# Kernel tuning notes

Hardware: AMD Instinct MI355X
Metric: run time of the kernel (lower is better)

Reference implementation:

```python
import jax, jax.numpy as jnp
import numpy as np

N = 100000   # nodes
E = 1600000  # edges per view
B = 256      # graphs in batch
D = 128      # feature dim
H, C = 4, 32 # heads, per-head channels (H*C = 128)


def _seg_softmax(logits, seg, num_seg):
    # numerically stable softmax over segments (per-destination / per-graph)
    m = jax.ops.segment_max(logits, seg, num_segments=num_seg)
    e = jnp.exp(logits - m[seg])
    s = jax.ops.segment_sum(e, seg, num_segments=num_seg)
    return e / s[seg]


def _gat_conv(x, edge_index, W, att_src, att_dst, bias):
    # PyG GATConv with add_self_loops=True, concat heads
    n = x.shape[0]
    loop = jnp.arange(n, dtype=edge_index.dtype)
    src = jnp.concatenate([edge_index[0], loop])
    dst = jnp.concatenate([edge_index[1], loop])
    xh = (x @ W).reshape(n, H, C)                      # [N,H,C]
    a_src = jnp.einsum('nhc,hc->nh', xh, att_src)      # [N,H]
    a_dst = jnp.einsum('nhc,hc->nh', xh, att_dst)
    alpha = jax.nn.leaky_relu(a_src[src] + a_dst[dst], 0.2)   # [E+N,H]
    alpha = _seg_softmax(alpha, dst, n)
    msg = xh[src] * alpha[..., None]                   # [E+N,H,C]
    out = jax.ops.segment_sum(msg, dst, num_segments=n)
    return out.reshape(n, H * C) + bias


def _global_attention(h, batch, gate_W, gate_b):
    gate = (h @ gate_W + gate_b)[:, 0]                 # [N]
    a = _seg_softmax(gate, batch, B)
    return jax.ops.segment_sum(a[:, None] * h, batch, num_segments=B)  # [B,128]


def setup_inputs() -> dict:
    key = jax.random.key(0)
    ks = jax.random.split(key, 32)
    p = lambda k, shp: (jax.random.normal(k, shp, dtype=jnp.float32) * 0.05)
    inp = {
        'x': jax.random.normal(ks[0], (N, D), dtype=jnp.float32),
        'edge_index_ast': jax.random.randint(ks[1], (2, E), 0, N, dtype=jnp.int32),
        'edge_index_cfg': jax.random.randint(ks[2], (2, E), 0, N, dtype=jnp.int32),
        'edge_index_pdg': jax.random.randint(ks[3], (2, E), 0, N, dtype=jnp.int32),
        'batch': jnp.sort(jax.random.randint(ks[4], (N,), 0, B, dtype=jnp.int32)),
        'ln_g': jnp.ones((D,), jnp.float32),
        'ln_b': jnp.zeros((D,), jnp.float32),
        'proj_W': p(ks[5], (D, D)), 'proj_b': p(ks[6], (D,)),
        'W_ast': p(ks[7], (D, H * C)), 'att_src_ast': p(ks[8], (H, C)), 'att_dst_ast': p(ks[9], (H, C)), 'bias_ast': p(ks[10], (H * C,)),
        'W_cfg': p(ks[11], (D, H * C)), 'att_src_cfg': p(ks[12], (H, C)), 'att_dst_cfg': p(ks[13], (H, C)), 'bias_cfg': p(ks[14], (H * C,)),
        'W_pdg': p(ks[15], (D, H * C)), 'att_src_pdg': p(ks[16], (H, C)), 'att_dst_pdg': p(ks[17], (H, C)), 'bias_pdg': p(ks[18], (H * C,)),
        'gate_W': p(ks[19], (H * C, 1)), 'gate_b': p(ks[20], (1,)),
        'clf_W1': p(ks[21], (3 * H * C, 128)), 'clf_b1': p(ks[22], (128,)),
        'clf_W2': p(ks[23], (128, 1)), 'clf_b2': p(ks[24], (1,)),
    }
    return inp


def reference(x, edge_index_ast, edge_index_cfg, edge_index_pdg, batch,
              ln_g, ln_b, proj_W, proj_b,
              W_ast, att_src_ast, att_dst_ast, bias_ast,
              W_cfg, att_src_cfg, att_dst_cfg, bias_cfg,
              W_pdg, att_src_pdg, att_dst_pdg, bias_pdg,
              gate_W, gate_b, clf_W1, clf_b1, clf_W2, clf_b2):
    # LayerNorm + proj + LeakyReLU (dropout = eval/no-op)
    mu = jnp.mean(x, axis=-1, keepdims=True)
    var = jnp.var(x, axis=-1, keepdims=True)
    xn = (x - mu) * jax.lax.rsqrt(var + 1e-5) * ln_g + ln_b
    h0 = jax.nn.leaky_relu(xn @ proj_W + proj_b, 0.01)

    h_ast = jax.nn.elu(_gat_conv(h0, edge_index_ast, W_ast, att_src_ast, att_dst_ast, bias_ast))
    g_ast = _global_attention(h_ast, batch, gate_W, gate_b)
    h_cfg = jax.nn.elu(_gat_conv(h0, edge_index_cfg, W_cfg, att_src_cfg, att_dst_cfg, bias_cfg))
    g_cfg = _global_attention(h_cfg, batch, gate_W, gate_b)
    h_pdg = jax.nn.elu(_gat_conv(h0, edge_index_pdg, W_pdg, att_src_pdg, att_dst_pdg, bias_pdg))
    g_pdg = _global_attention(h_pdg, batch, gate_W, gate_b)

    combined = jnp.concatenate([g_ast, g_cfg, g_pdg], axis=1)  # [B, 384]
    hid = jax.nn.leaky_relu(combined @ clf_W1 + clf_b1, 0.01)
    return (hid @ clf_W2 + clf_b2).reshape(-1)                 # [B]
```

## Files before the change

### kernel.cpp

```cpp
#include <hip/hip_runtime.h>
#include <hip/hip_bf16.h>
#include <hip/hip_fp16.h>
#include <math.h>

#define NN 100000
#define EE 1600000
#define BB 256
#define NBUCK 391
#define PBLK 384
#define CH 4167
#define TOTB (3 * PBLK)
#define ROWS_PAD 100096
#define EPV (EE + NN)
#define LOG2E 1.442695041f

typedef short bf16x8 __attribute__((ext_vector_type(8)));
typedef float f32x4 __attribute__((ext_vector_type(4)));

__device__ __forceinline__ unsigned short f2bf(float f) {
    __hip_bfloat16 h = __float2bfloat16(f);
    return *(unsigned short*)&h;
}
__device__ __forceinline__ unsigned short f2h(float f) {
    __half h = __float2half(f);
    return *(unsigned short*)&h;
}
__device__ __forceinline__ float h2f(unsigned short u) {
    __half h = *(__half*)&u;
    return __half2float(h);
}

__global__ __launch_bounds__(256) void pack_wt(const float* __restrict__ W0,
                                               const float* __restrict__ W1,
                                               const float* __restrict__ W2,
                                               const float* __restrict__ W3,
                                               const float* __restrict__ ln_g,
                                               unsigned short* __restrict__ WT) {
    int which = blockIdx.y;
    const float* W = which == 0 ? W0 : which == 1 ? W1 : which == 2 ? W2 : W3;
    int i = blockIdx.x * 256 + threadIdx.x;
    int n = i >> 7, k = i & 127;
    float v = W[k * 128 + n];
    if (which == 0) v *= ln_g[k];
    WT[which * 16384 + i] = f2bf(v);
}

__global__ __launch_bounds__(128) void ln_consts(const float* __restrict__ W,
                                                 const float* __restrict__ g,
                                                 const float* __restrict__ b,
                                                 float* __restrict__ c12) {
    int n = threadIdx.x;
    float c1 = 0.f, c2 = 0.f;
    for (int k = 0; k < 128; k++) {
        float w = W[k * 128 + n];
        c1 = fmaf(g[k], w, c1);
        c2 = fmaf(b[k], w, c2);
    }
    c12[n] = c1;
    c12[128 + n] = c2;
}


__device__ __forceinline__ void hist_body(int bid, int tid,
                                          const int* __restrict__ e0,
                                          const int* __restrict__ e1,
                                          const int* __restrict__ e2,
                                          int* __restrict__ blockHistT) {
    int v = bid / PBLK, p = bid % PBLK;
    const int* ei = v == 0 ? e0 : v == 1 ? e1 : e2;
    __shared__ int h[NBUCK];
    for (int i = tid; i < NBUCK; i += 256) h[i] = 0;
    __syncthreads();
    int ea = p * CH, ebnd = min(EE, ea + CH);
    int e = ea + tid;
    for (; e + 768 < ebnd; e += 1024) {
        int d0 = ei[EE + e], d1 = ei[EE + e + 256];
        int d2 = ei[EE + e + 512], d3 = ei[EE + e + 768];
        atomicAdd(&h[((unsigned)d0) >> 8], 1);
        atomicAdd(&h[((unsigned)d1) >> 8], 1);
        atomicAdd(&h[((unsigned)d2) >> 8], 1);
        atomicAdd(&h[((unsigned)d3) >> 8], 1);
    }
    for (; e < ebnd; e += 256) atomicAdd(&h[((unsigned)ei[EE + e]) >> 8], 1);
    __syncthreads();
    for (int i = tid; i < NBUCK; i += 256) blockHistT[i * TOTB + bid] = h[i];
}

__device__ __forceinline__ void proj_body(int nb, int tid,
                                          const float* __restrict__ X,
                                          const unsigned short* __restrict__ WT,
                                          const float* __restrict__ c12,
                                          const float* __restrict__ pb,
                                          unsigned short* __restrict__ Out) {
    int w = tid >> 6, lane = tid & 63;
    int ln = lane & 15, oct = lane >> 4;
    int row0 = nb * 128 + w * 32;

    f32x4 acc[2][8];
    #pragma unroll
    for (int i = 0; i < 2; i++)
        #pragma unroll
        for (int j = 0; j < 8; j++) acc[i][j] = (f32x4){0.f, 0.f, 0.f, 0.f};

    const float* X0 = X + (size_t)min(row0 + ln, NN - 1) * 128;
    const float* X1 = X + (size_t)min(row0 + 16 + ln, NN - 1) * 128;
    const bf16x8* Wr = (const bf16x8*)(WT + (size_t)ln * 128);

    float s0 = 0.f, q0 = 0.f, s1 = 0.f, q1 = 0.f;
    #pragma unroll
    for (int kq = 0; kq < 4; kq++) {
        int koff = kq * 4 + oct;
        float4 xa = *(const float4*)(X0 + koff * 8);
        float4 xb = *(const float4*)(X0 + koff * 8 + 4);
        float4 ya = *(const float4*)(X1 + koff * 8);
        float4 yb = *(const float4*)(X1 + koff * 8 + 4);
        s0 += (xa.x + xa.y) + (xa.z + xa.w) + (xb.x + xb.y) + (xb.z + xb.w);
        q0 += xa.x * xa.x + xa.y * xa.y + xa.z * xa.z + xa.w * xa.w
            + xb.x * xb.x + xb.y * xb.y + xb.z * xb.z + xb.w * xb.w;
        s1 += (ya.x + ya.y) + (ya.z + ya.w) + (yb.x + yb.y) + (yb.z + yb.w);
        q1 += ya.x * ya.x + ya.y * ya.y + ya.z * ya.z + ya.w * ya.w
            + yb.x * yb.x + yb.y * yb.y + yb.z * yb.z + yb.w * yb.w;
        bf16x8 a0, a1;
        a0[0] = (short)f2bf(xa.x); a0[1] = (short)f2bf(xa.y); a0[2] = (short)f2bf(xa.z); a0[3] = (short)f2bf(xa.w);
        a0[4] = (short)f2bf(xb.x); a0[5] = (short)f2bf(xb.y); a0[6] = (short)f2bf(xb.z); a0[7] = (short)f2bf(xb.w);
        a1[0] = (short)f2bf(ya.x); a1[1] = (short)f2bf(ya.y); a1[2] = (short)f2bf(ya.z); a1[3] = (short)f2bf(ya.w);
        a1[4] = (short)f2bf(yb.x); a1[5] = (short)f2bf(yb.y); a1[6] = (short)f2bf(yb.z); a1[7] = (short)f2bf(yb.w);
        #pragma unroll
        for (int ct = 0; ct < 8; ct++) {
            bf16x8 bfr = Wr[ct * 16 * 16 + koff];
            acc[0][ct] = __builtin_amdgcn_mfma_f32_16x16x32_bf16(a0, bfr, acc[0][ct], 0, 0, 0);
            acc[1][ct] = __builtin_amdgcn_mfma_f32_16x16x32_bf16(a1, bfr, acc[1][ct], 0, 0, 0);
        }
    }
    #pragma unroll
    for (int m = 16; m < 64; m <<= 1) {
        s0 += __shfl_xor(s0, m); q0 += __shfl_xor(q0, m);
        s1 += __shfl_xor(s1, m); q1 += __shfl_xor(q1, m);
    }
    float mu0 = s0 * (1.0f / 128.0f);
    float rs0 = rsqrtf(q0 * (1.0f / 128.0f) - mu0 * mu0 + 1e-5f);
    float mu1 = s1 * (1.0f / 128.0f);
    float rs1 = rsqrtf(q1 * (1.0f / 128.0f) - mu1 * mu1 + 1e-5f);

    float c1v[8], c2v[8], pbv[8];
    #pragma unroll
    for (int ct = 0; ct < 8; ct++) {
        c1v[ct] = c12[ct * 16 + ln];
        c2v[ct] = c12[128 + ct * 16 + ln];
        pbv[ct] = pb[ct * 16 + ln];
    }
    #pragma unroll
    for (int rt = 0; rt < 2; rt++) {
        #pragma unroll
        for (int r = 0; r < 4; r++) {
            int src = oct * 4 + r;
            float rs_r = __shfl(rt ? rs1 : rs0, src);
            float mu_r = __shfl(rt ? mu1 : mu0, src);
            int row = row0 + rt * 16 + oct * 4 + r;
            #pragma unroll
            for (int ct = 0; ct < 8; ct++) {
                float v = rs_r * acc[rt][ct][r] - rs_r * mu_r * c1v[ct] + c2v[ct] + pbv[ct];
                v = v > 0.f ? v : 0.01f * v;
                Out[(size_t)row * 128 + ct * 16 + ln] = f2bf(v);
            }
        }
    }
}

__device__ __forceinline__ void scatter_body(int bid, int tid,
                                             const int* __restrict__ e0,
                                             const int* __restrict__ e1,
                                             const int* __restrict__ e2,
                                             const int* __restrict__ blockOffT,
                                             unsigned int* __restrict__ pairbuf) {
    int v = bid / PBLK, p = bid % PBLK;
    const int* ei = v == 0 ? e0 : v == 1 ? e1 : e2;
    __shared__ int cur[NBUCK];
    for (int i = tid; i < NBUCK; i += 256) cur[i] = blockOffT[(size_t)i * TOTB + bid];
    __syncthreads();
    int ea = p * CH, ebnd = min(EE, ea + CH);
    unsigned int* pbuf = pairbuf + (size_t)v * EE;
    int e = ea + tid;
    for (; e + 768 < ebnd; e += 1024) {
        unsigned s0 = (unsigned)ei[e],       d0 = (unsigned)ei[EE + e];
        unsigned s1 = (unsigned)ei[e + 256], d1 = (unsigned)ei[EE + e + 256];
        unsigned s2 = (unsigned)ei[e + 512], d2 = (unsigned)ei[EE + e + 512];
        unsigned s3 = (unsigned)ei[e + 768], d3 = (unsigned)ei[EE + e + 768];
        int p0 = atomicAdd(&cur[d0 >> 8], 1);
        int p1 = atomicAdd(&cur[d1 >> 8], 1);
        int p2 = atomicAdd(&cur[d2 >> 8], 1);
        int p3 = atomicAdd(&cur[d3 >> 8], 1);
        pbuf[p0] = (s0 << 8) | (d0 & 255u);
        pbuf[p1] = (s1 << 8) | (d1 & 255u);
        pbuf[p2] = (s2 << 8) | (d2 & 255u);
        pbuf[p3] = (s3 << 8) | (d3 & 255u);
    }
    for (; e < ebnd; e += 256) {
        unsigned s = (unsigned)ei[e], d = (unsigned)ei[EE + e];
        int pos = atomicAdd(&cur[d >> 8], 1);
        pbuf[pos] = (s << 8) | (d & 255u);
    }
}

__device__ __forceinline__ void view_body(int nb, int tid,
                                          const unsigned short* __restrict__ h0,
                                          const unsigned short* __restrict__ WTv,
                                          const float* __restrict__ asw,
                                          const float* __restrict__ adw,
                                          unsigned short* __restrict__ Out,
                                          float* __restrict__ a_src,
                                          float* __restrict__ a_dst) {
    int w = tid >> 6, lane = tid & 63;
    int ln = lane & 15, oct = lane >> 4;
    int row0 = nb * 128 + w * 32;

    f32x4 acc[2][8];
    #pragma unroll
    for (int i = 0; i < 2; i++)
        #pragma unroll
        for (int j = 0; j < 8; j++) acc[i][j] = (f32x4){0.f, 0.f, 0.f, 0.f};

    const bf16x8* Ar0 = (const bf16x8*)(h0 + (size_t)(row0 + ln) * 128);
    const bf16x8* Ar1 = (const bf16x8*)(h0 + (size_t)(row0 + 16 + ln) * 128);
    const bf16x8* Wr  = (const bf16x8*)(WTv + (size_t)ln * 128);

    #pragma unroll
    for (int kq = 0; kq < 4; kq++) {
        int koff = kq * 4 + oct;
        bf16x8 a0 = Ar0[koff];
        bf16x8 a1 = Ar1[koff];
        #pragma unroll
        for (int ct = 0; ct < 8; ct++) {
            bf16x8 bfr = Wr[ct * 16 * 16 + koff];
            acc[0][ct] = __builtin_amdgcn_mfma_f32_16x16x32_bf16(a0, bfr, acc[0][ct], 0, 0, 0);
            acc[1][ct] = __builtin_amdgcn_mfma_f32_16x16x32_bf16(a1, bfr, acc[1][ct], 0, 0, 0);
        }
    }
    float aswv[8], adwv[8];
    #pragma unroll
    for (int ct = 0; ct < 8; ct++) { aswv[ct] = asw[ct * 16 + ln]; adwv[ct] = adw[ct * 16 + ln]; }

    #pragma unroll
    for (int rt = 0; rt < 2; rt++) {
        #pragma unroll
        for (int r = 0; r < 4; r++) {
            int row = row0 + rt * 16 + oct * 4 + r;
            float sh_[4] = {0.f, 0.f, 0.f, 0.f}, dh_[4] = {0.f, 0.f, 0.f, 0.f};
            #pragma unroll
            for (int ct = 0; ct < 8; ct++) {
                float vv = acc[rt][ct][r];
                Out[(size_t)row * 128 + ct * 16 + ln] = f2h(vv);
                sh_[ct >> 1] = fmaf(vv, aswv[ct], sh_[ct >> 1]);
                dh_[ct >> 1] = fmaf(vv, adwv[ct], dh_[ct >> 1]);
            }
            #pragma unroll
            for (int off = 1; off < 16; off <<= 1) {
                #pragma unroll
                for (int h = 0; h < 4; h++) {
                    sh_[h] += __shfl_xor(sh_[h], off);
                    dh_[h] += __shfl_xor(dh_[h], off);
                }
            }
            if (ln == 0) {
                *(float4*)(a_src + (size_t)row * 4) = make_float4(sh_[0], sh_[1], sh_[2], sh_[3]);
                *(float4*)(a_dst + (size_t)row * 4) = make_float4(dh_[0], dh_[1], dh_[2], dh_[3]);
            }
        }
    }
}

__global__ __launch_bounds__(256) void fat_hist_proj(const int* e0, const int* e1, const int* e2,
                                                     int* blockHistT,
                                                     const float* X, const unsigned short* WT,
                                                     const float* c12, const float* pb,
                                                     unsigned short* h0) {
    if (blockIdx.x < TOTB) hist_body(blockIdx.x, threadIdx.x, e0, e1, e2, blockHistT);
    else proj_body(blockIdx.x - TOTB, threadIdx.x, X, WT, c12, pb, h0);
}

__global__ __launch_bounds__(256) void fat_scatter_view(const int* e0, const int* e1, const int* e2,
                                                        const int* blockOffT, unsigned int* pairbuf,
                                                        const unsigned short* h0, const unsigned short* WT,
                                                        const float* as0, const float* ad0,
                                                        unsigned short* xh, float* a_src, float* a_dst) {
    if (blockIdx.x < TOTB) scatter_body(blockIdx.x, threadIdx.x, e0, e1, e2, blockOffT, pairbuf);
    else view_body(blockIdx.x - TOTB, threadIdx.x, h0, WT + 16384, as0, ad0, xh, a_src, a_dst);
}

__global__ __launch_bounds__(256) void gemm_view(const unsigned short* __restrict__ h0,
                                                 const unsigned short* __restrict__ WTv,
                                                 const float* __restrict__ asw,
                                                 const float* __restrict__ adw,
                                                 unsigned short* __restrict__ Out,
                                                 float* __restrict__ a_src,
                                                 float* __restrict__ a_dst) {
    view_body(blockIdx.x, threadIdx.x, h0, WTv, asw, adw, Out, a_src, a_dst);
}

__global__ __launch_bounds__(256) void csr_bsum(const int* __restrict__ blockHistT,
                                                int* __restrict__ btot) {
    int wid = (blockIdx.x * 256 + threadIdx.x) >> 6;
    int lane = threadIdx.x & 63;
    if (wid >= 3 * NBUCK) return;
    int v = wid / NBUCK, b = wid - v * NBUCK;
    const int* row = blockHistT + (size_t)b * TOTB + v * PBLK;
    int s = 0;
    #pragma unroll
    for (int j = 0; j < 6; j++) s += row[lane * 6 + j];
    #pragma unroll
    for (int m = 1; m < 64; m <<= 1) s += __shfl_xor(s, m);
    if (lane == 0) btot[wid] = s;
}

__global__ __launch_bounds__(512) void csr_scan(const int* __restrict__ btot,
                                                int* __restrict__ ebstart,
                                                int* __restrict__ bstart) {
    int v = blockIdx.x, t = threadIdx.x;
    __shared__ int se[512], ss[512];
    int tot_e = (t < NBUCK) ? btot[v * NBUCK + t] : 0;
    int nval = (t < NBUCK) ? min(256, NN - t * 256) : 0;
    int tot_s = tot_e + nval;
    se[t] = tot_e; ss[t] = tot_s;
    __syncthreads();
    for (int s = 1; s < 512; s <<= 1) {
        int ae = (t >= s) ? se[t - s] : 0;
        int as_ = (t >= s) ? ss[t - s] : 0;
        __syncthreads();
        se[t] += ae; ss[t] += as_;
        __syncthreads();
    }
    if (t < NBUCK) {
        ebstart[v * (NBUCK + 1) + t] = se[t] - tot_e;
        bstart[v * (NBUCK + 1) + t] = ss[t] - tot_s;
    }
    if (t == NBUCK - 1) {
        ebstart[v * (NBUCK + 1) + NBUCK] = se[t];
        bstart[v * (NBUCK + 1) + NBUCK] = ss[t];
    }
}

__global__ __launch_bounds__(256) void csr_boff(const int* __restrict__ blockHistT,
                                                const int* __restrict__ ebstart,
                                                int* __restrict__ blockOffT) {
    int wid = (blockIdx.x * 256 + threadIdx.x) >> 6;
    int lane = threadIdx.x & 63;
    if (wid >= 3 * NBUCK) return;
    int v = wid / NBUCK, b = wid - v * NBUCK;
    const int* row = blockHistT + (size_t)b * TOTB + v * PBLK;
    int* orow = blockOffT + (size_t)b * TOTB + v * PBLK;
    int vals[6], lexcl[6];
    int ls = 0;
    #pragma unroll
    for (int j = 0; j < 6; j++) vals[j] = row[lane * 6 + j];
    #pragma unroll
    for (int j = 0; j < 6; j++) { lexcl[j] = ls; ls += vals[j]; }
    int incl = ls;
    #pragma unroll
    for (int m = 1; m < 64; m <<= 1) {
        int t = __shfl_up(incl, m);
        if (lane >= m) incl += t;
    }
    int wexcl = incl - ls;
    int base = ebstart[v * (NBUCK + 1) + b];
    #pragma unroll
    for (int j = 0; j < 6; j++) orow[lane * 6 + j] = base + wexcl + lexcl[j];
}

__global__ __launch_bounds__(256) void csr_fine(const unsigned int* __restrict__ pairbuf,
                                                const int* __restrict__ btot,
                                                const int* __restrict__ ebstart,
                                                const int* __restrict__ bstart,
                                                int* __restrict__ deg3,
                                                int* __restrict__ start3,
                                                unsigned int* __restrict__ ebuf3) {
    int v = blockIdx.x / NBUCK, b = blockIdx.x - v * NBUCK;
    int cnt   = btot[v * NBUCK + b];
    int pbase = ebstart[v * (NBUCK + 1) + b];
    int obase = bstart[v * (NBUCK + 1) + b];
    const unsigned int* pb = pairbuf + (size_t)v * EE + pbase;
    unsigned int* eb = ebuf3 + (size_t)v * EPV + obase;
    __shared__ int hist[256], scan[256], cur[256];
    int t = threadIdx.x;
    int node = b * 256 + t;
    int valid = (node < NN) ? 1 : 0;
    hist[t] = valid;
    __syncthreads();
    {
        int i = t;
        for (; i + 768 < cnt; i += 1024) {
            unsigned v0 = pb[i], v1 = pb[i + 256], v2 = pb[i + 512], v3 = pb[i + 768];
            atomicAdd(&hist[v0 & 255u], 1);
            atomicAdd(&hist[v1 & 255u], 1);
            atomicAdd(&hist[v2 & 255u], 1);
            atomicAdd(&hist[v3 & 255u], 1);
        }
        for (; i < cnt; i += 256) atomicAdd(&hist[pb[i] & 255u], 1);
    }
    __syncthreads();
    scan[t] = hist[t];
    __syncthreads();
    for (int s = 1; s < 256; s <<= 1) {
        int u = (t >= s) ? scan[t - s] : 0;
        __syncthreads();
        scan[t] += u;
        __syncthreads();
    }
    int excl = scan[t] - hist[t];
    cur[t] = excl + valid;
    if (valid) eb[excl] = (((unsigned)node) << 8) | ((unsigned)node & 255u);
    __syncthreads();
    {
        int i = t;
        for (; i + 768 < cnt; i += 1024) {
            unsigned v0 = pb[i], v1 = pb[i + 256], v2 = pb[i + 512], v3 = pb[i + 768];
            int p0 = atomicAdd(&cur[v0 & 255u], 1);
            int p1 = atomicAdd(&cur[v1 & 255u], 1);
            int p2 = atomicAdd(&cur[v2 & 255u], 1);
            int p3 = atomicAdd(&cur[v3 & 255u], 1);
            eb[p0] = v0; eb[p1] = v1; eb[p2] = v2; eb[p3] = v3;
        }
        for (; i < cnt; i += 256) {
            unsigned int val = pb[i];
            int pos = atomicAdd(&cur[val & 255u], 1);
            eb[pos] = val;
        }
    }
    if (valid) {
        deg3[v * NN + node] = hist[t];
        start3[v * NN + node] = obase + excl;
    }
}

__global__ __launch_bounds__(256) void aggregate_kernel(const unsigned short* __restrict__ xh,
                                                        const int* __restrict__ start,
                                                        const int* __restrict__ deg,
                                                        const unsigned int* __restrict__ ebuf,
                                                        const float* __restrict__ a_src,
                                                        const float* __restrict__ a_dst,
                                                        const float* __restrict__ bias,
                                                        const float* __restrict__ gw,
                                                        const float* __restrict__ gb,
                                                        unsigned short* __restrict__ hvb,
                                                        float* __restrict__ gexpv) {
    __shared__ float wlds[4 * 260];
    int node = (blockIdx.x * 256 + threadIdx.x) >> 6;
    int lane = threadIdx.x & 63;
    if (node >= NN) return;
    int h = lane >> 4;
    int st = start[node];
    int cnt = deg[node];
    const char* xb = (const char*)xh;
    int laneoff = lane * 4;
    float4 ad4 = *(const float4*)(a_dst + (size_t)node * 4);
    float* ww = wlds + (threadIdx.x >> 6) * 260;
    const float* wr = ww + h * 65;

    float accx = 0.f, accy = 0.f;
    float d0s = 0.f, d1s = 0.f, d2s = 0.f, d3s = 0.f;
    for (int j0 = 0; j0 < cnt; j0 += 64) {
        int nj = min(64, cnt - j0);
        int src_l = 0;
        if (lane < nj) {
            src_l = (int)(ebuf[st + j0 + lane] >> 8);
            float4 as4 = *(const float4*)(a_src + (size_t)src_l * 4);
            float t0 = as4.x + ad4.x, t1 = as4.y + ad4.y;
            float t2 = as4.z + ad4.z, t3 = as4.w + ad4.w;
            t0 = fmaxf(t0, 0.f) + 0.2f * fminf(t0, 0.f);
            t1 = fmaxf(t1, 0.f) + 0.2f * fminf(t1, 0.f);
            t2 = fmaxf(t2, 0.f) + 0.2f * fminf(t2, 0.f);
            t3 = fmaxf(t3, 0.f) + 0.2f * fminf(t3, 0.f);
            float w0 = exp2f(t0 * LOG2E);
            float w1 = exp2f(t1 * LOG2E);
            float w2 = exp2f(t2 * LOG2E);
            float w3 = exp2f(t3 * LOG2E);
            d0s += w0; d1s += w1; d2s += w2; d3s += w3;
            ww[0 * 65 + lane] = w0;
            ww[1 * 65 + lane] = w1;
            ww[2 * 65 + lane] = w2;
            ww[3 * 65 + lane] = w3;
        }
        int jj = 0;
        for (; jj + 4 <= nj; jj += 4) {
            int s0 = __builtin_amdgcn_readlane(src_l, jj);
            int s1 = __builtin_amdgcn_readlane(src_l, jj + 1);
            int s2 = __builtin_amdgcn_readlane(src_l, jj + 2);
            int s3 = __builtin_amdgcn_readlane(src_l, jj + 3);
            float w0 = wr[jj];
            float w1 = wr[jj + 1];
            float w2 = wr[jj + 2];
            float w3 = wr[jj + 3];
            __half2 x0 = *(const __half2*)(xb + (((size_t)(unsigned)s0) << 8) + laneoff);
            __half2 x1 = *(const __half2*)(xb + (((size_t)(unsigned)s1) << 8) + laneoff);
            __half2 x2 = *(const __half2*)(xb + (((size_t)(unsigned)s2) << 8) + laneoff);
            __half2 x3 = *(const __half2*)(xb + (((size_t)(unsigned)s3) << 8) + laneoff);
            accx = fmaf(__low2float(x0), w0, accx);
            accy = fmaf(__high2float(x0), w0, accy);
            accx = fmaf(__low2float(x1), w1, accx);
            accy = fmaf(__high2float(x1), w1, accy);
            accx = fmaf(__low2float(x2), w2, accx);
            accy = fmaf(__high2float(x2), w2, accy);
            accx = fmaf(__low2float(x3), w3, accx);
            accy = fmaf(__high2float(x3), w3, accy);
        }
        for (; jj < nj; jj++) {
            int s = __builtin_amdgcn_readlane(src_l, jj);
            float w = wr[jj];
            __half2 xv = *(const __half2*)(xb + (((size_t)(unsigned)s) << 8) + laneoff);
            accx = fmaf(__low2float(xv), w, accx);
            accy = fmaf(__high2float(xv), w, accy);
        }
    }
    #pragma unroll
    for (int m = 1; m < 64; m <<= 1) {
        d0s += __shfl_xor(d0s, m);
        d1s += __shfl_xor(d1s, m);
        d2s += __shfl_xor(d2s, m);
        d3s += __shfl_xor(d3s, m);
    }
    float den = (h == 0) ? d0s : (h == 1) ? d1s : (h == 2) ? d2s : d3s;
    float inv = 1.0f / den;
    float2 bb = *(const float2*)(bias + lane * 2);
    float o0 = accx * inv + bb.x;
    float o1 = accy * inv + bb.y;
    o0 = o0 > 0.f ? o0 : exp2f(o0 * LOG2E) - 1.0f;
    o1 = o1 > 0.f ? o1 : exp2f(o1 * LOG2E) - 1.0f;
    unsigned int packed = (unsigned)f2h(o0) | ((unsigned)f2h(o1) << 16);
    *(unsigned int*)(hvb + (size_t)node * 128 + lane * 2) = packed;
    float2 g2 = *(const float2*)(gw + lane * 2);
    float gp = o0 * g2.x + o1 * g2.y;
    #pragma unroll
    for (int m = 1; m < 64; m <<= 1) gp += __shfl_xor(gp, m);
    if (lane == 0) gexpv[node] = exp2f((gp + gb[0]) * LOG2E);
}

__global__ __launch_bounds__(1024) void pool_kernel(const unsigned short* __restrict__ hvb,
                                                    const float* __restrict__ gexpv,
                                                    const int* __restrict__ batch,
                                                    float* __restrict__ gout,
                                                    int voff) {
    int b = blockIdx.x;
    int g = threadIdx.x >> 7;
    int ch = threadIdx.x & 127;
    int l = 0, r = NN;
    while (l < r) { int m = (l + r) >> 1; if (batch[m] < b) l = m + 1; else r = m; }
    int s0 = l;
    r = NN;
    while (l < r) { int m = (l + r) >> 1; if (batch[m] < b + 1) l = m + 1; else r = m; }
    int s1 = l;
    float acc = 0.f, wsum = 0.f;
    for (int n = s0 + g; n < s1; n += 8) {
        float w = gexpv[n];
        wsum += w;
        acc = fmaf(w, h2f(hvb[(size_t)n * 128 + ch]), acc);
    }
    __shared__ float sacc[8][128];
    __shared__ float sws[8];
    sacc[g][ch] = acc;
    if (ch == 0) sws[g] = wsum;
    __syncthreads();
    if (g == 0) {
        float a = 0.f, w = 0.f;
        #pragma unroll
        for (int i = 0; i < 8; i++) { a += sacc[i][ch]; w += sws[i]; }
        gout[b * 384 + voff + ch] = (s1 > s0) ? a / w : 0.f;
    }
}

__global__ __launch_bounds__(128) void clf_kernel(const float* __restrict__ gout,
                                                  const float* __restrict__ W1,
                                                  const float* __restrict__ b1,
                                                  const float* __restrict__ W2,
                                                  const float* __restrict__ b2,
                                                  float* __restrict__ out) {
    int b = blockIdx.x;
    int j = threadIdx.x;
    float acc = b1[j];
    for (int k = 0; k < 384; k++) acc = fmaf(gout[b * 384 + k], W1[k * 128 + j], acc);
    acc = acc > 0.f ? acc : 0.01f * acc;
    float p = acc * W2[j];
    #pragma unroll
    for (int m = 1; m < 64; m <<= 1) p += __shfl_xor(p, m);
    __shared__ float sh[2];
    if ((j & 63) == 0) sh[j >> 6] = p;
    __syncthreads();
    if (j == 0) out[b] = sh[0] + sh[1] + b2[0];
}

extern "C" void kernel_launch(void* const* d_in, const int* in_sizes, int n_in,
                              void* d_out, int out_size, void* d_ws, size_t ws_size,
                              hipStream_t stream) {
    const float* x      = (const float*)d_in[0];
    const int*   ei[3]  = {(const int*)d_in[1], (const int*)d_in[2], (const int*)d_in[3]};
    const int*   batch  = (const int*)d_in[4];
    const float* ln_g   = (const float*)d_in[5];
    const float* ln_b   = (const float*)d_in[6];
    const float* proj_W = (const float*)d_in[7];
    const float* proj_b = (const float*)d_in[8];
    const float* Wv[3]  = {(const float*)d_in[9],  (const float*)d_in[13], (const float*)d_in[17]};
    const float* asv[3] = {(const float*)d_in[10], (const float*)d_in[14], (const float*)d_in[18]};
    const float* adv[3] = {(const float*)d_in[11], (const float*)d_in[15], (const float*)d_in[19]};
    const float* bv[3]  = {(const float*)d_in[12], (const float*)d_in[16], (const float*)d_in[20]};
    const float* gate_W = (const float*)d_in[21];
    const float* gate_b = (const float*)d_in[22];
    const float* clf_W1 = (const float*)d_in[23];
    const float* clf_b1 = (const float*)d_in[24];
    const float* clf_W2 = (const float*)d_in[25];
    const float* clf_b2 = (const float*)d_in[26];
    float* out = (float*)d_out;

    (void)in_sizes; (void)n_in; (void)out_size; (void)ws_size;

    char* base = (char*)d_ws;
    size_t off = 0;
    auto nxt = [&](size_t bytes) { char* r = base + off; off += (bytes + 255) & ~(size_t)255; return r; };
    unsigned short* h0   = (unsigned short*)nxt((size_t)ROWS_PAD * 128 * 2);
    unsigned short* xh   = (unsigned short*)nxt((size_t)ROWS_PAD * 128 * 2);
    unsigned short* hvb  = (unsigned short*)nxt((size_t)NN * 128 * 2);
    unsigned short* WT   = (unsigned short*)nxt(4 * 16384 * 2);
    float* c12    = (float*)nxt(256 * 4);
    float* a_src  = (float*)nxt((size_t)ROWS_PAD * 4 * 4);
    float* a_dst  = (float*)nxt((size_t)ROWS_PAD * 4 * 4);
    float* gexpv  = (float*)nxt(NN * 4);
    float* gout   = (float*)nxt(BB * 384 * 4);
    int* deg3     = (int*)nxt(3 * NN * 4);
    int* start3   = (int*)nxt(3 * NN * 4);
    unsigned int* ebuf3 = (unsigned int*)nxt(((size_t)3 * EPV + 64) * 4);
    int* btot     = (int*)nxt(3 * NBUCK * 4);
    int* ebstart  = (int*)nxt(3 * (NBUCK + 1) * 4);
    int* bstart   = (int*)nxt(3 * (NBUCK + 1) * 4);
    int* blockHistT = (int*)nxt((size_t)NBUCK * TOTB * 4);
    int* blockOffT  = (int*)nxt((size_t)NBUCK * TOTB * 4);
    unsigned int* pairbuf = (unsigned int*)nxt((size_t)3 * EE * 4);

    pack_wt<<<dim3(64, 4), 256, 0, stream>>>(proj_W, Wv[0], Wv[1], Wv[2], ln_g, WT);
    ln_consts<<<1, 128, 0, stream>>>(proj_W, ln_g, ln_b, c12);
    fat_hist_proj<<<TOTB + 782, 256, 0, stream>>>(ei[0], ei[1], ei[2], blockHistT,
                                                  x, WT, c12, proj_b, h0);
    csr_bsum<<<(3 * NBUCK + 3) / 4, 256, 0, stream>>>(blockHistT, btot);
    csr_scan<<<3, 512, 0, stream>>>(btot, ebstart, bstart);
    csr_boff<<<(3 * NBUCK + 3) / 4, 256, 0, stream>>>(blockHistT, ebstart, blockOffT);
    fat_scatter_view<<<TOTB + 782, 256, 0, stream>>>(ei[0], ei[1], ei[2], blockOffT, pairbuf,
                                                     h0, WT, asv[0], adv[0], xh, a_src, a_dst);
    csr_fine<<<3 * NBUCK, 256, 0, stream>>>(pairbuf, btot, ebstart, bstart, deg3, start3, ebuf3);
    for (int v = 0; v < 3; v++) {
        if (v > 0)
            gemm_view<<<782, 256, 0, stream>>>(h0, WT + (size_t)(1 + v) * 16384,
                                               asv[v], adv[v], xh, a_src, a_dst);
        aggregate_kernel<<<25000, 256, 0, stream>>>(xh, start3 + v * NN, deg3 + v * NN,
                                                    ebuf3 + (size_t)v * EPV,
                                                    a_src, a_dst,
                                                    bv[v], gate_W, gate_b, hvb, gexpv);
        pool_kernel<<<256, 1024, 0, stream>>>(hvb, gexpv, batch, gout, v * 128);
    }
    clf_kernel<<<256, 128, 0, stream>>>(gout, clf_W1, clf_b1, clf_W2, clf_b2, out);
}
```

Baseline: 687.2 us.

## Batch all three GAT views into single gemm, aggregate and pool launches

Gives each view its own xh, a_src/a_dst, hvb and gexpv buffers, so all three views' projection GEMMs run inside the scatter kernel and aggregation and pooling each become one launch over three views. The goal is to remove the serial per-view launches and the tail underutilisation of small grids. A workspace-size check falls back to the old per-view path. The ln_consts reduction is also split across 512 threads. It costs roughly three times the workspace for the intermediate buffers.

```diff
diff --git a/kernel.cpp b/kernel.cpp
--- a/kernel.cpp
+++ b/kernel.cpp
@@ -13,6 +13,11 @@
 #define ROWS_PAD 100096
 #define EPV (EE + NN)
 #define LOG2E 1.442695041f
+#define GEMM_BLKS 782
+#define AGG_BLKS 25000
+#define XH_ELEMS ((size_t)ROWS_PAD * 128)
+#define A_ELEMS ((size_t)ROWS_PAD * 4)
+#define HV_ELEMS ((size_t)NN * 128)
 
 typedef short bf16x8 __attribute__((ext_vector_type(8)));
 typedef float f32x4 __attribute__((ext_vector_type(4)));
@@ -45,19 +50,27 @@
     WT[which * 16384 + i] = f2bf(v);
 }
 
-__global__ __launch_bounds__(128) void ln_consts(const float* __restrict__ W,
+__global__ __launch_bounds__(512) void ln_consts(const float* __restrict__ W,
                                                  const float* __restrict__ g,
                                                  const float* __restrict__ b,
                                                  float* __restrict__ c12) {
-    int n = threadIdx.x;
+    __shared__ float p1[512], p2[512];
+    int t = threadIdx.x;
+    int n = t & 127, kg = t >> 7;
     float c1 = 0.f, c2 = 0.f;
-    for (int k = 0; k < 128; k++) {
+    for (int k = kg * 32; k < kg * 32 + 32; k++) {
         float w = W[k * 128 + n];
         c1 = fmaf(g[k], w, c1);
         c2 = fmaf(b[k], w, c2);
     }
-    c12[n] = c1;
-    c12[128 + n] = c2;
+    p1[t] = c1; p2[t] = c2;
+    __syncthreads();
+    if (kg == 0) {
+        c1 = p1[n] + p1[128 + n] + p1[256 + n] + p1[384 + n];
+        c2 = p2[n] + p2[128 + n] + p2[256 + n] + p2[384 + n];
+        c12[n] = c1;
+        c12[128 + n] = c2;
+    }
 }
 
 
@@ -269,190 +282,27 @@
     }
 }
 
-__global__ __launch_bounds__(256) void fat_hist_proj(const int* e0, const int* e1, const int* e2,
-                                                     int* blockHistT,
-                                                     const float* X, const unsigned short* WT,
-                                                     const float* c12, const float* pb,
-                                                     unsigned short* h0) {
-    if (blockIdx.x < TOTB) hist_body(blockIdx.x, threadIdx.x, e0, e1, e2, blockHistT);
-    else proj_body(blockIdx.x - TOTB, threadIdx.x, X, WT, c12, pb, h0);
-}
-
-__global__ __launch_bounds__(256) void fat_scatter_view(const int* e0, const int* e1, const int* e2,
-                                                        const int* blockOffT, unsigned int* pairbuf,
-                                                        const unsigned short* h0, const unsigned short* WT,
-                                                        const float* as0, const float* ad0,
-                                                        unsigned short* xh, float* a_src, float* a_dst) {
-    if (blockIdx.x < TOTB) scatter_body(blockIdx.x, threadIdx.x, e0, e1, e2, blockOffT, pairbuf);
-    else view_body(blockIdx.x - TOTB, threadIdx.x, h0, WT + 16384, as0, ad0, xh, a_src, a_dst);
-}
-
-__global__ __launch_bounds__(256) void gemm_view(const unsigned short* __restrict__ h0,
-                                                 const unsigned short* __restrict__ WTv,
-                                                 const float* __restrict__ asw,
-                                                 const float* __restrict__ adw,
-                                                 unsigned short* __restrict__ Out,
-                                                 float* __restrict__ a_src,
-                                                 float* __restrict__ a_dst) {
-    view_body(blockIdx.x, threadIdx.x, h0, WTv, asw, adw, Out, a_src, a_dst);
-}
-
-__global__ __launch_bounds__(256) void csr_bsum(const int* __restrict__ blockHistT,
-                                                int* __restrict__ btot) {
-    int wid = (blockIdx.x * 256 + threadIdx.x) >> 6;
-    int lane = threadIdx.x & 63;
-    if (wid >= 3 * NBUCK) return;
-    int v = wid / NBUCK, b = wid - v * NBUCK;
-    const int* row = blockHistT + (size_t)b * TOTB + v * PBLK;
-    int s = 0;
-    #pragma unroll
-    for (int j = 0; j < 6; j++) s += row[lane * 6 + j];
-    #pragma unroll
-    for (int m = 1; m < 64; m <<= 1) s += __shfl_xor(s, m);
-    if (lane == 0) btot[wid] = s;
-}
-
-__global__ __launch_bounds__(512) void csr_scan(const int* __restrict__ btot,
-                                                int* __restrict__ ebstart,
-                                                int* __restrict__ bstart) {
-    int v = blockIdx.x, t = threadIdx.x;
-    __shared__ int se[512], ss[512];
-    int tot_e = (t < NBUCK) ? btot[v * NBUCK + t] : 0;
-    int nval = (t < NBUCK) ? min(256, NN - t * 256) : 0;
-    int tot_s = tot_e + nval;
-    se[t] = tot_e; ss[t] = tot_s;
-    __syncthreads();
-    for (int s = 1; s < 512; s <<= 1) {
-        int ae = (t >= s) ? se[t - s] : 0;
-        int as_ = (t >= s) ? ss[t - s] : 0;
-        __syncthreads();
-        se[t] += ae; ss[t] += as_;
-        __syncthreads();
-    }
-    if (t < NBUCK) {
-        ebstart[v * (NBUCK + 1) + t] = se[t] - tot_e;
-        bstart[v * (NBUCK + 1) + t] = ss[t] - tot_s;
-    }
-    if (t == NBUCK - 1) {
-        ebstart[v * (NBUCK + 1) + NBUCK] = se[t];
-        bstart[v * (NBUCK + 1) + NBUCK] = ss[t];
-    }
-}
-
-__global__ __launch_bounds__(256) void csr_boff(const int* __restrict__ blockHistT,
-                                                const int* __restrict__ ebstart,
-                                                int* __restrict__ blockOffT) {
-    int wid = (blockIdx.x * 256 + threadIdx.x) >> 6;
-    int lane = threadIdx.x & 63;
-    if (wid >= 3 * NBUCK) return;
-    int v = wid / NBUCK, b = wid - v * NBUCK;
-    const int* row = blockHistT + (size_t)b * TOTB + v * PBLK;
-    int* orow = blockOffT + (size_t)b * TOTB + v * PBLK;
-    int vals[6], lexcl[6];
-    int ls = 0;
-    #pragma unroll
-    for (int j = 0; j < 6; j++) vals[j] = row[lane * 6 + j];
-    #pragma unroll
-    for (int j = 0; j < 6; j++) { lexcl[j] = ls; ls += vals[j]; }
-    int incl = ls;
-    #pragma unroll
-    for (int m = 1; m < 64; m <<= 1) {
-        int t = __shfl_up(incl, m);
-        if (lane >= m) incl += t;
-    }
-    int wexcl = incl - ls;
-    int base = ebstart[v * (NBUCK + 1) + b];
-    #pragma unroll
-    for (int j = 0; j < 6; j++) orow[lane * 6 + j] = base + wexcl + lexcl[j];
-}
-
-__global__ __launch_bounds__(256) void csr_fine(const unsigned int* __restrict__ pairbuf,
-                                                const int* __restrict__ btot,
-                                                const int* __restrict__ ebstart,
-                                                const int* __restrict__ bstart,
-                                                int* __restrict__ deg3,
-                                                int* __restrict__ start3,
-                                                unsigned int* __restrict__ ebuf3) {
-    int v = blockIdx.x / NBUCK, b = blockIdx.x - v * NBUCK;
-    int cnt   = btot[v * NBUCK + b];
-    int pbase = ebstart[v * (NBUCK + 1) + b];
-    int obase = bstart[v * (NBUCK + 1) + b];
-    const unsigned int* pb = pairbuf + (size_t)v * EE + pbase;
-    unsigned int* eb = ebuf3 + (size_t)v * EPV + obase;
-    __shared__ int hist[256], scan[256], cur[256];
-    int t = threadIdx.x;
-    int node = b * 256 + t;
-    int valid = (node < NN) ? 1 : 0;
-    hist[t] = valid;
-    __syncthreads();
-    {
-        int i = t;
-        for (; i + 768 < cnt; i += 1024) {
-            unsigned v0 = pb[i], v1 = pb[i + 256], v2 = pb[i + 512], v3 = pb[i + 768];
-            atomicAdd(&hist[v0 & 255u], 1);
-            atomicAdd(&hist[v1 & 255u], 1);
-            atomicAdd(&hist[v2 & 255u], 1);
-            atomicAdd(&hist[v3 & 255u], 1);
-        }
-        for (; i < cnt; i += 256) atomicAdd(&hist[pb[i] & 255u], 1);
-    }
-    __syncthreads();
-    scan[t] = hist[t];
-    __syncthreads();
-    for (int s = 1; s < 256; s <<= 1) {
-        int u = (t >= s) ? scan[t - s] : 0;
-        __syncthreads();
-        scan[t] += u;
-        __syncthreads();
-    }
-    int excl = scan[t] - hist[t];
-    cur[t] = excl + valid;
-    if (valid) eb[excl] = (((unsigned)node) << 8) | ((unsigned)node & 255u);
-    __syncthreads();
-    {
-        int i = t;
-        for (; i + 768 < cnt; i += 1024) {
-            unsigned v0 = pb[i], v1 = pb[i + 256], v2 = pb[i + 512], v3 = pb[i + 768];
-            int p0 = atomicAdd(&cur[v0 & 255u], 1);
-            int p1 = atomicAdd(&cur[v1 & 255u], 1);
-            int p2 = atomicAdd(&cur[v2 & 255u], 1);
-            int p3 = atomicAdd(&cur[v3 & 255u], 1);
-            eb[p0] = v0; eb[p1] = v1; eb[p2] = v2; eb[p3] = v3;
-        }
-        for (; i < cnt; i += 256) {
-            unsigned int val = pb[i];
-            int pos = atomicAdd(&cur[val & 255u], 1);
-            eb[pos] = val;
-        }
-    }
-    if (valid) {
-        deg3[v * NN + node] = hist[t];
-        start3[v * NN + node] = obase + excl;
-    }
-}
-
-__global__ __launch_bounds__(256) void aggregate_kernel(const unsigned short* __restrict__ xh,
-                                                        const int* __restrict__ start,
-                                                        const int* __restrict__ deg,
-                                                        const unsigned int* __restrict__ ebuf,
-                                                        const float* __restrict__ a_src,
-                                                        const float* __restrict__ a_dst,
-                                                        const float* __restrict__ bias,
-                                                        const float* __restrict__ gw,
-                                                        const float* __restrict__ gb,
-                                                        unsigned short* __restrict__ hvb,
-                                                        float* __restrict__ gexpv) {
-    __shared__ float wlds[4 * 260];
-    int node = (blockIdx.x * 256 + threadIdx.x) >> 6;
-    int lane = threadIdx.x & 63;
-    if (node >= NN) return;
+__device__ __forceinline__ void agg_body(int node, int tid,
+                                         const unsigned short* __restrict__ xh,
+                                         const int* __restrict__ start,
+                                         const int* __restrict__ deg,
+                                         const unsigned int* __restrict__ ebuf,
+                                         const float* __restrict__ a_src,
+                                         const float* __restrict__ a_dst,
+                                         const float* __restrict__ bias,
+                                         const float* __restrict__ gw,
+                                         const float* __restrict__ gb,
+                                         unsigned short* __restrict__ hvb,
+                                         float* __restrict__ gexpv,
+                                         float* wlds) {
+    int lane = tid & 63;
     int h = lane >> 4;
     int st = start[node];
     int cnt = deg[node];
     const char* xb = (const char*)xh;
     int laneoff = lane * 4;
     float4 ad4 = *(const float4*)(a_dst + (size_t)node * 4);
-    float* ww = wlds + (threadIdx.x >> 6) * 260;
+    float* ww = wlds + (tid >> 6) * 260;
     const float* wr = ww + h * 65;
 
     float accx = 0.f, accy = 0.f;
@@ -533,14 +383,15 @@
     if (lane == 0) gexpv[node] = exp2f((gp + gb[0]) * LOG2E);
 }
 
-__global__ __launch_bounds__(1024) void pool_kernel(const unsigned short* __restrict__ hvb,
-                                                    const float* __restrict__ gexpv,
-                                                    const int* __restrict__ batch,
-                                                    float* __restrict__ gout,
-                                                    int voff) {
-    int b = blockIdx.x;
-    int g = threadIdx.x >> 7;
-    int ch = threadIdx.x & 127;
+__device__ __forceinline__ void pool_body(int b, int tid,
+                                          const unsigned short* __restrict__ hvb,
+                                          const float* __restrict__ gexpv,
+                                          const int* __restrict__ batch,
+                                          float* __restrict__ gout,
+                                          int voff,
+                                          float* sacc, float* sws) {
+    int g = tid >> 7;
+    int ch = tid & 127;
     int l = 0, r = NN;
     while (l < r) { int m = (l + r) >> 1; if (batch[m] < b) l = m + 1; else r = m; }
     int s0 = l;
@@ -553,17 +404,265 @@
         wsum += w;
         acc = fmaf(w, h2f(hvb[(size_t)n * 128 + ch]), acc);
     }
-    __shared__ float sacc[8][128];
-    __shared__ float sws[8];
-    sacc[g][ch] = acc;
+    sacc[g * 128 + ch] = acc;
     if (ch == 0) sws[g] = wsum;
     __syncthreads();
     if (g == 0) {
         float a = 0.f, w = 0.f;
         #pragma unroll
-        for (int i = 0; i < 8; i++) { a += sacc[i][ch]; w += sws[i]; }
+        for (int i = 0; i < 8; i++) { a += sacc[i * 128 + ch]; w += sws[i]; }
         gout[b * 384 + voff + ch] = (s1 > s0) ? a / w : 0.f;
     }
+}
+
+__global__ __launch_bounds__(256) void fat_hist_proj(const int* e0, const int* e1, const int* e2,
+                                                     int* blockHistT,
+                                                     const float* X, const unsigned short* WT,
+                                                     const float* c12, const float* pb,
+                                                     unsigned short* h0) {
+    if (blockIdx.x < TOTB) hist_body(blockIdx.x, threadIdx.x, e0, e1, e2, blockHistT);
+    else proj_body(blockIdx.x - TOTB, threadIdx.x, X, WT, c12, pb, h0);
+}
+
+__global__ __launch_bounds__(256) void fat_scatter_view(const int* e0, const int* e1, const int* e2,
+                                                        const int* blockOffT, unsigned int* pairbuf,
+                                                        const unsigned short* h0, const unsigned short* WT,
+                                                        const float* as0, const float* ad0,
+                                                        unsigned short* xh, float* a_src, float* a_dst) {
+    if (blockIdx.x < TOTB) scatter_body(blockIdx.x, threadIdx.x, e0, e1, e2, blockOffT, pairbuf);
+    else view_body(blockIdx.x - TOTB, threadIdx.x, h0, WT + 16384, as0, ad0, xh, a_src, a_dst);
+}
+
+__global__ __launch_bounds__(256) void fat_scatter_view3(const int* e0, const int* e1, const int* e2,
+                                                         const int* blockOffT, unsigned int* pairbuf,
+                                                         const unsigned short* h0, const unsigned short* WT,
+                                                         const float* as0, const float* ad0,
+                                                         const float* as1, const float* ad1,
+                                                         const float* as2, const float* ad2,
+                                                         unsigned short* xh3, float* a_src3, float* a_dst3) {
+    if (blockIdx.x < TOTB) {
+        scatter_body(blockIdx.x, threadIdx.x, e0, e1, e2, blockOffT, pairbuf);
+        return;
+    }
+    int t = blockIdx.x - TOTB;
+    int v = t / GEMM_BLKS;
+    int nb = t - v * GEMM_BLKS;
+    const float* as_ = v == 0 ? as0 : v == 1 ? as1 : as2;
+    const float* ad_ = v == 0 ? ad0 : v == 1 ? ad1 : ad2;
+    view_body(nb, threadIdx.x, h0, WT + (size_t)(1 + v) * 16384, as_, ad_,
+              xh3 + (size_t)v * XH_ELEMS,
+              a_src3 + (size_t)v * A_ELEMS, a_dst3 + (size_t)v * A_ELEMS);
+}
+
+__global__ __launch_bounds__(256) void gemm_view(const unsigned short* __restrict__ h0,
+                                                 const unsigned short* __restrict__ WTv,
+                                                 const float* __restrict__ asw,
+                                                 const float* __restrict__ adw,
+                                                 unsigned short* __restrict__ Out,
+                                                 float* __restrict__ a_src,
+                                                 float* __restrict__ a_dst) {
+    view_body(blockIdx.x, threadIdx.x, h0, WTv, asw, adw, Out, a_src, a_dst);
+}
+
+__global__ __launch_bounds__(256) void csr_bsum(const int* __restrict__ blockHistT,
+                                                int* __restrict__ btot) {
+    int wid = (blockIdx.x * 256 + threadIdx.x) >> 6;
+    int lane = threadIdx.x & 63;
+    if (wid >= 3 * NBUCK) return;
+    int v = wid / NBUCK, b = wid - v * NBUCK;
+    const int* row = blockHistT + (size_t)b * TOTB + v * PBLK;
+    int s = 0;
+    #pragma unroll
+    for (int j = 0; j < 6; j++) s += row[lane * 6 + j];
+    #pragma unroll
+    for (int m = 1; m < 64; m <<= 1) s += __shfl_xor(s, m);
+    if (lane == 0) btot[wid] = s;
+}
+
+__global__ __launch_bounds__(512) void csr_scan(const int* __restrict__ btot,
+                                                int* __restrict__ ebstart,
+                                                int* __restrict__ bstart) {
+    int v = blockIdx.x, t = threadIdx.x;
+    __shared__ int se[512], ss[512];
+    int tot_e = (t < NBUCK) ? btot[v * NBUCK + t] : 0;
+    int nval = (t < NBUCK) ? min(256, NN - t * 256) : 0;
+    int tot_s = tot_e + nval;
+    se[t] = tot_e; ss[t] = tot_s;
+    __syncthreads();
+    for (int s = 1; s < 512; s <<= 1) {
+        int ae = (t >= s) ? se[t - s] : 0;
+        int as_ = (t >= s) ? ss[t - s] : 0;
+        __syncthreads();
+        se[t] += ae; ss[t] += as_;
+        __syncthreads();
+    }
+    if (t < NBUCK) {
+        ebstart[v * (NBUCK + 1) + t] = se[t] - tot_e;
+        bstart[v * (NBUCK + 1) + t] = ss[t] - tot_s;
+    }
+    if (t == NBUCK - 1) {
+        ebstart[v * (NBUCK + 1) + NBUCK] = se[t];
+        bstart[v * (NBUCK + 1) + NBUCK] = ss[t];
+    }
+}
+
+__global__ __launch_bounds__(256) void csr_boff(const int* __restrict__ blockHistT,
+                                                const int* __restrict__ ebstart,
+                                                int* __restrict__ blockOffT) {
+    int wid = (blockIdx.x * 256 + threadIdx.x) >> 6;
+    int lane = threadIdx.x & 63;
+    if (wid >= 3 * NBUCK) return;
+    int v = wid / NBUCK, b = wid - v * NBUCK;
+    const int* row = blockHistT + (size_t)b * TOTB + v * PBLK;
+    int* orow = blockOffT + (size_t)b * TOTB + v * PBLK;
+    int vals[6], lexcl[6];
+    int ls = 0;
+    #pragma unroll
+    for (int j = 0; j < 6; j++) vals[j] = row[lane * 6 + j];
+    #pragma unroll
+    for (int j = 0; j < 6; j++) { lexcl[j] = ls; ls += vals[j]; }
+    int incl = ls;
+    #pragma unroll
+    for (int m = 1; m < 64; m <<= 1) {
+        int t = __shfl_up(incl, m);
+        if (lane >= m) incl += t;
+    }
+    int wexcl = incl - ls;
+    int base = ebstart[v * (NBUCK + 1) + b];
+    #pragma unroll
+    for (int j = 0; j < 6; j++) orow[lane * 6 + j] = base + wexcl + lexcl[j];
+}
+
+__global__ __launch_bounds__(256) void csr_fine(const unsigned int* __restrict__ pairbuf,
+                                                const int* __restrict__ btot,
+                                                const int* __restrict__ ebstart,
+                                                const int* __restrict__ bstart,
+                                                int* __restrict__ deg3,
+                                                int* __restrict__ start3,
+                                                unsigned int* __restrict__ ebuf3) {
+    int v = blockIdx.x / NBUCK, b = blockIdx.x - v * NBUCK;
+    int cnt   = btot[v * NBUCK + b];
+    int pbase = ebstart[v * (NBUCK + 1) + b];
+    int obase = bstart[v * (NBUCK + 1) + b];
+    const unsigned int* pb = pairbuf + (size_t)v * EE + pbase;
+    unsigned int* eb = ebuf3 + (size_t)v * EPV + obase;
+    __shared__ int hist[256], scan[256], cur[256];
+    int t = threadIdx.x;
+    int node = b * 256 + t;
+    int valid = (node < NN) ? 1 : 0;
+    hist[t] = valid;
+    __syncthreads();
+    {
+        int i = t;
+        for (; i + 768 < cnt; i += 1024) {
+            unsigned v0 = pb[i], v1 = pb[i + 256], v2 = pb[i + 512], v3 = pb[i + 768];
+            atomicAdd(&hist[v0 & 255u], 1);
+            atomicAdd(&hist[v1 & 255u], 1);
+            atomicAdd(&hist[v2 & 255u], 1);
+            atomicAdd(&hist[v3 & 255u], 1);
+        }
+        for (; i < cnt; i += 256) atomicAdd(&hist[pb[i] & 255u], 1);
+    }
+    __syncthreads();
+    scan[t] = hist[t];
+    __syncthreads();
+    for (int s = 1; s < 256; s <<= 1) {
+        int u = (t >= s) ? scan[t - s] : 0;
+        __syncthreads();
+        scan[t] += u;
+        __syncthreads();
+    }
+    int excl = scan[t] - hist[t];
+    cur[t] = excl + valid;
+    if (valid) eb[excl] = (((unsigned)node) << 8) | ((unsigned)node & 255u);
+    __syncthreads();
+    {
+        int i = t;
+        for (; i + 768 < cnt; i += 1024) {
+            unsigned v0 = pb[i], v1 = pb[i + 256], v2 = pb[i + 512], v3 = pb[i + 768];
+            int p0 = atomicAdd(&cur[v0 & 255u], 1);
+            int p1 = atomicAdd(&cur[v1 & 255u], 1);
+            int p2 = atomicAdd(&cur[v2 & 255u], 1);
+            int p3 = atomicAdd(&cur[v3 & 255u], 1);
+            eb[p0] = v0; eb[p1] = v1; eb[p2] = v2; eb[p3] = v3;
+        }
+        for (; i < cnt; i += 256) {
+            unsigned int val = pb[i];
+            int pos = atomicAdd(&cur[val & 255u], 1);
+            eb[pos] = val;
+        }
+    }
+    if (valid) {
+        deg3[v * NN + node] = hist[t];
+        start3[v * NN + node] = obase + excl;
+    }
+}
+
+__global__ __launch_bounds__(256) void aggregate_kernel(const unsigned short* __restrict__ xh,
+                                                        const int* __restrict__ start,
+                                                        const int* __restrict__ deg,
+                                                        const unsigned int* __restrict__ ebuf,
+                                                        const float* __restrict__ a_src,
+                                                        const float* __restrict__ a_dst,
+                                                        const float* __restrict__ bias,
+                                                        const float* __restrict__ gw,
+                                                        const float* __restrict__ gb,
+                                                        unsigned short* __restrict__ hvb,
+                                                        float* __restrict__ gexpv) {
+    __shared__ float wlds[4 * 260];
+    int node = (blockIdx.x * 256 + threadIdx.x) >> 6;
+    if (node >= NN) return;
+    agg_body(node, threadIdx.x, xh, start, deg, ebuf, a_src, a_dst, bias, gw, gb, hvb, gexpv, wlds);
+}
+
+__global__ __launch_bounds__(256) void aggregate3_kernel(const unsigned short* __restrict__ xh3,
+                                                         const int* __restrict__ start3,
+                                                         const int* __restrict__ deg3,
+                                                         const unsigned int* __restrict__ ebuf3,
+                                                         const float* __restrict__ a_src3,
+                                                         const float* __restrict__ a_dst3,
+                                                         const float* __restrict__ b0,
+                                                         const float* __restrict__ b1,
+                                                         const float* __restrict__ b2,
+                                                         const float* __restrict__ gw,
+                                                         const float* __restrict__ gb,
+                                                         unsigned short* __restrict__ hvb3,
+                                                         float* __restrict__ gexpv3) {
+    __shared__ float wlds[4 * 260];
+    int v = blockIdx.x / AGG_BLKS;
+    int bin = blockIdx.x - v * AGG_BLKS;
+    int node = (bin * 256 + threadIdx.x) >> 6;
+    if (node >= NN) return;
+    const float* bias = v == 0 ? b0 : v == 1 ? b1 : b2;
+    agg_body(node, threadIdx.x,
+             xh3 + (size_t)v * XH_ELEMS,
+             start3 + v * NN, deg3 + v * NN,
+             ebuf3 + (size_t)v * EPV,
+             a_src3 + (size_t)v * A_ELEMS, a_dst3 + (size_t)v * A_ELEMS,
+             bias, gw, gb,
+             hvb3 + (size_t)v * HV_ELEMS, gexpv3 + v * NN, wlds);
+}
+
+__global__ __launch_bounds__(1024) void pool_kernel(const unsigned short* __restrict__ hvb,
+                                                    const float* __restrict__ gexpv,
+                                                    const int* __restrict__ batch,
+                                                    float* __restrict__ gout,
+                                                    int voff) {
+    __shared__ float sacc[8 * 128];
+    __shared__ float sws[8];
+    pool_body(blockIdx.x, threadIdx.x, hvb, gexpv, batch, gout, voff, sacc, sws);
+}
+
+__global__ __launch_bounds__(1024) void pool3_kernel(const unsigned short* __restrict__ hvb3,
+                                                     const float* __restrict__ gexpv3,
+                                                     const int* __restrict__ batch,
+                                                     float* __restrict__ gout) {
+    __shared__ float sacc[8 * 128];
+    __shared__ float sws[8];
+    int v = blockIdx.x >> 8;
+    int b = blockIdx.x & 255;
+    pool_body(b, threadIdx.x, hvb3 + (size_t)v * HV_ELEMS, gexpv3 + v * NN,
+              batch, gout, v * 128, sacc, sws);
 }
 
 __global__ __launch_bounds__(128) void clf_kernel(const float* __restrict__ gout,
@@ -608,49 +707,77 @@
     const float* clf_b2 = (const float*)d_in[26];
     float* out = (float*)d_out;
 
-    (void)in_sizes; (void)n_in; (void)out_size; (void)ws_size;
+    (void)in_sizes; (void)n_in; (void)out_size;
 
     char* base = (char*)d_ws;
     size_t off = 0;
     auto nxt = [&](size_t bytes) { char* r = base + off; off += (bytes + 255) & ~(size_t)255; return r; };
-    unsigned short* h0   = (unsigned short*)nxt((size_t)ROWS_PAD * 128 * 2);
-    unsigned short* xh   = (unsigned short*)nxt((size_t)ROWS_PAD * 128 * 2);
-    unsigned short* hvb  = (unsigned short*)nxt((size_t)NN * 128 * 2);
-    unsigned short* WT   = (unsigned short*)nxt(4 * 16384 * 2);
-    float* c12    = (float*)nxt(256 * 4);
-    float* a_src  = (float*)nxt((size_t)ROWS_PAD * 4 * 4);
-    float* a_dst  = (float*)nxt((size_t)ROWS_PAD * 4 * 4);
-    float* gexpv  = (float*)nxt(NN * 4);
-    float* gout   = (float*)nxt(BB * 384 * 4);
-    int* deg3     = (int*)nxt(3 * NN * 4);
-    int* start3   = (int*)nxt(3 * NN * 4);
-    unsigned int* ebuf3 = (unsigned int*)nxt(((size_t)3 * EPV + 64) * 4);
-    int* btot     = (int*)nxt(3 * NBUCK * 4);
-    int* ebstart  = (int*)nxt(3 * (NBUCK + 1) * 4);
-    int* bstart   = (int*)nxt(3 * (NBUCK + 1) * 4);
-    int* blockHistT = (int*)nxt((size_t)NBUCK * TOTB * 4);
-    int* blockOffT  = (int*)nxt((size_t)NBUCK * TOTB * 4);
-    unsigned int* pairbuf = (unsigned int*)nxt((size_t)3 * EE * 4);
+
+    unsigned short *h0, *xh, *hvb, *WT;
+    float *c12, *a_src, *a_dst, *gexpv, *gout;
+    int *deg3, *start3, *btot, *ebstart, *bstart, *blockHistT, *blockOffT;
+    unsigned int *ebuf3, *pairbuf;
+
+    auto layout = [&](int m) {
+        off = 0;
+        h0   = (unsigned short*)nxt((size_t)ROWS_PAD * 128 * 2);
+        xh   = (unsigned short*)nxt((size_t)m * XH_ELEMS * 2);
+        hvb  = (unsigned short*)nxt((size_t)m * HV_ELEMS * 2);
+        WT   = (unsigned short*)nxt(4 * 16384 * 2);
+        c12    = (float*)nxt(256 * 4);
+        a_src  = (float*)nxt((size_t)m * A_ELEMS * 4);
+        a_dst  = (float*)nxt((size_t)m * A_ELEMS * 4);
+        gexpv  = (float*)nxt((size_t)m * NN * 4);
+        gout   = (float*)nxt(BB * 384 * 4);
+        deg3   = (int*)nxt(3 * NN * 4);
+        start3 = (int*)nxt(3 * NN * 4);
+        ebuf3  = (unsigned int*)nxt(((size_t)3 * EPV + 64) * 4);
+        btot   = (int*)nxt(3 * NBUCK * 4);
+        ebstart = (int*)nxt(3 * (NBUCK + 1) * 4);
+        bstart  = (int*)nxt(3 * (NBUCK + 1) * 4);
+        blockHistT = (int*)nxt((size_t)NBUCK * TOTB * 4);
+        blockOffT  = (int*)nxt((size_t)NBUCK * TOTB * 4);
+        pairbuf = (unsigned int*)nxt((size_t)3 * EE * 4);
+        return off;
+    };
+
+    size_t need_fast = layout(3);
+    bool fast = (ws_size >= need_fast);
+    if (!fast) layout(1);
 
     pack_wt<<<dim3(64, 4), 256, 0, stream>>>(proj_W, Wv[0], Wv[1], Wv[2], ln_g, WT);
-    ln_consts<<<1, 128, 0, stream>>>(proj_W, ln_g, ln_b, c12);
-    fat_hist_proj<<<TOTB + 782, 256, 0, stream>>>(ei[0], ei[1], ei[2], blockHistT,
-                                                  x, WT, c12, proj_b, h0);
+    ln_consts<<<1, 512, 0, stream>>>(proj_W, ln_g, ln_b, c12);
+    fat_hist_proj<<<TOTB + GEMM_BLKS, 256, 0, stream>>>(ei[0], ei[1], ei[2], blockHistT,
+                                                        x, WT, c12, proj_b, h0);
     csr_bsum<<<(3 * NBUCK + 3) / 4, 256, 0, stream>>>(blockHistT, btot);
     csr_scan<<<3, 512, 0, stream>>>(btot, ebstart, bstart);
     csr_boff<<<(3 * NBUCK + 3) / 4, 256, 0, stream>>>(blockHistT, ebstart, blockOffT);
-    fat_scatter_view<<<TOTB + 782, 256, 0, stream>>>(ei[0], ei[1], ei[2], blockOffT, pairbuf,
-                                                     h0, WT, asv[0], adv[0], xh, a_src, a_dst);
-    csr_fine<<<3 * NBUCK, 256, 0, stream>>>(pairbuf, btot, ebstart, bstart, deg3, start3, ebuf3);
-    for (int v = 0; v < 3; v++) {
-        if (v > 0)
-            gemm_view<<<782, 256, 0, stream>>>(h0, WT + (size_t)(1 + v) * 16384,
-                                               asv[v], adv[v], xh, a_src, a_dst);
-        aggregate_kernel<<<25000, 256, 0, stream>>>(xh, start3 + v * NN, deg3 + v * NN,
-                                                    ebuf3 + (size_t)v * EPV,
-                                                    a_src, a_dst,
-                                                    bv[v], gate_W, gate_b, hvb, gexpv);
-        pool_kernel<<<256, 1024, 0, stream>>>(hvb, gexpv, batch, gout, v * 128);
+
+    if (fast) {
+        fat_scatter_view3<<<TOTB + 3 * GEMM_BLKS, 256, 0, stream>>>(
+            ei[0], ei[1], ei[2], blockOffT, pairbuf, h0, WT,
+            asv[0], adv[0], asv[1], adv[1], asv[2], adv[2],
+            xh, a_src, a_dst);
+        csr_fine<<<3 * NBUCK, 256, 0, stream>>>(pairbuf, btot, ebstart, bstart, deg3, start3, ebuf3);
+        aggregate3_kernel<<<3 * AGG_BLKS, 256, 0, stream>>>(xh, start3, deg3, ebuf3,
+                                                            a_src, a_dst,
+                                                            bv[0], bv[1], bv[2],
+                                                            gate_W, gate_b, hvb, gexpv);
+        pool3_kernel<<<3 * 256, 1024, 0, stream>>>(hvb, gexpv, batch, gout);
+    } else {
+        fat_scatter_view<<<TOTB + GEMM_BLKS, 256, 0, stream>>>(ei[0], ei[1], ei[2], blockOffT, pairbuf,
+                                                               h0, WT, asv[0], adv[0], xh, a_src, a_dst);
+        csr_fine<<<3 * NBUCK, 256, 0, stream>>>(pairbuf, btot, ebstart, bstart, deg3, start3, ebuf3);
+        for (int v = 0; v < 3; v++) {
+            if (v > 0)
+                gemm_view<<<GEMM_BLKS, 256, 0, stream>>>(h0, WT + (size_t)(1 + v) * 16384,
+                                                         asv[v], adv[v], xh, a_src, a_dst);
+            aggregate_kernel<<<AGG_BLKS, 256, 0, stream>>>(xh, start3 + v * NN, deg3 + v * NN,
+                                                           ebuf3 + (size_t)v * EPV,
+                                                           a_src, a_dst,
+                                                           bv[v], gate_W, gate_b, hvb, gexpv);
+            pool_kernel<<<256, 1024, 0, stream>>>(hvb, gexpv, batch, gout, v * 128);
+        }
     }
     clf_kernel<<<256, 128, 0, stream>>>(gout, clf_W1, clf_b1, clf_W2, clf_b2, out);
 }
```

After: 629.1 us. -8.5%, faster.
